# Optimization experiments

Measured on AMD Instinct MI355X. Metric: run time of the kernel, lower is better.

## Reference

```python
import jax, jax.numpy as jnp
import numpy as np

B, N, M, DQ, DK, DV, H = 8, 1024, 1024, 512, 512, 512, 8
DS = DV // H  # dim_split = 64
NEG = -1e38


def _ln(x, g, b, eps=1e-5):
    mu = jnp.mean(x, -1, keepdims=True)
    var = jnp.mean((x - mu) ** 2, -1, keepdims=True)
    return (x - mu) * jax.lax.rsqrt(var + eps) * g + b


def setup_inputs() -> dict:
    key = jax.random.key(0)
    ks = jax.random.split(key, 16)
    s = 0.02
    return {
        "x": jax.random.normal(ks[0], (B, N, DQ), jnp.float32),
        "y": jax.random.normal(ks[1], (B, M, DK), jnp.float32),
        "x_mask": jax.random.randint(ks[2], (B, N), 0, 2).astype(bool),
        "y_mask": jax.random.randint(ks[3], (B, M), 0, 2).astype(bool),
        "Wq": jax.random.normal(ks[4], (DQ, DV), jnp.float32) * s,
        "Wk": jax.random.normal(ks[5], (DK, DV), jnp.float32) * s,
        "Wv": jax.random.normal(ks[6], (DK, DV), jnp.float32) * s,
        "Wo": jax.random.normal(ks[7], (DV, DQ), jnp.float32) * s,
        "W1": jax.random.normal(ks[8], (DQ, DQ), jnp.float32) * s,
        "b1": jnp.zeros((DQ,), jnp.float32),
        "W2": jax.random.normal(ks[9], (DQ, DQ), jnp.float32) * s,
        "b2": jnp.zeros((DQ,), jnp.float32),
        "g1": jnp.ones((DQ,), jnp.float32),
        "be1": jnp.zeros((DQ,), jnp.float32),
        "g2": jnp.ones((DQ,), jnp.float32),
        "be2": jnp.zeros((DQ,), jnp.float32),
    }


def reference(x, y, x_mask, y_mask, Wq, Wk, Wv, Wo, W1, b1, W2, b2, g1, be1, g2, be2):
    xm = x_mask[..., None]  # [B,N,1]
    ym = y_mask[..., None]  # [B,M,1]
    x = jnp.where(xm, 0.0, x)
    y = jnp.where(ym, 0.0, y)
    # projections (no bias); masked rows stay zero, re-mask as in source
    q = jnp.where(xm, 0.0, x @ Wq).reshape(B, N, H, DS)
    k = jnp.where(ym, 0.0, y @ Wk).reshape(B, M, H, DS)
    v = jnp.where(ym, 0.0, y @ Wv).reshape(B, M, H, DS)
    # scaled dot product; NOTE: scale is sqrt(dim_v), faithful to source
    sdp = jnp.einsum('bnhd,bmhd->bhnm', q, k) / np.sqrt(DV)
    mask = x_mask[:, None, :, None] | y_mask[:, None, None, :]  # [B,1,N,M]
    sdp = jnp.where(mask, NEG, sdp)
    alpha = jax.nn.softmax(sdp, axis=-1)  # softmax over keys (slot_att=False)
    att = jnp.einsum('bhnm,bmhd->bnhd', alpha, v).reshape(B, N, DV)
    att = jnp.where(xm, 0.0, att)
    o = x + att @ Wo
    o = _ln(o, g1, be1)
    ff = jax.nn.relu(o @ W1 + b1) @ W2 + b2
    o = _ln(o + ff, g2, be2)
    return jnp.where(xm, 0.0, o)
```

## Files before the change

kernel.cpp:

```cpp
#include <hip/hip_runtime.h>
#include <hip/hip_bf16.h>

typedef __bf16 bf16;
typedef __attribute__((ext_vector_type(4))) __bf16 bf16x4;
typedef __attribute__((ext_vector_type(8))) __bf16 bf16x8;
typedef __attribute__((ext_vector_type(4))) float f32x4;

#define B_ 8
#define N_ 1024
#define M_ 1024
#define H_ 8
#define ROWS_ (B_ * N_)

__device__ __forceinline__ f32x4 mfma16(bf16x8 a, bf16x8 b, f32x4 c) {
    return __builtin_amdgcn_mfma_f32_16x16x32_bf16(a, b, c, 0, 0, 0);
}

__device__ __forceinline__ void glds16(const void* g, void* l) {
    __builtin_amdgcn_global_load_lds((const __attribute__((address_space(1))) void*)g,
                                     (__attribute__((address_space(3))) void*)l, 16, 0, 0);
}

__global__ __launch_bounds__(256) void prep(const float* __restrict__ x, const float* __restrict__ y,
                                            bf16* __restrict__ Xb, bf16* __restrict__ Yb,
                                            const float* W0, const float* W1, const float* W2,
                                            const float* W3, const float* W4, const float* W5,
                                            bf16* T0, bf16* T1, bf16* T2, bf16* T3, bf16* T4, bf16* T5) {
    __shared__ float t[64][65];
    int bid = blockIdx.x;
    if (bid < 8192) {
        int i = bid * 256 + threadIdx.x;
        const float4* s;
        bf16x4* d;
        int j;
        if (i < 1048576) { s = (const float4*)x; d = (bf16x4*)Xb; j = i; }
        else             { s = (const float4*)y; d = (bf16x4*)Yb; j = i - 1048576; }
        float4 f = s[j];
        bf16x4 o = {(bf16)f.x, (bf16)f.y, (bf16)f.z, (bf16)f.w};
        d[j] = o;
        return;
    }
    int wb = bid - 8192;
    const float* srcs[6] = {W0, W1, W2, W3, W4, W5};
    bf16* dsts[6] = {T0, T1, T2, T3, T4, T5};
    const float* W = srcs[wb >> 6];
    bf16* Wt = dsts[wb >> 6];
    int tile = wb & 63;
    int k0 = (tile >> 3) * 64, n0 = (tile & 7) * 64;
    int tx = threadIdx.x & 63, ty = threadIdx.x >> 6;
#pragma unroll
    for (int j = 0; j < 16; ++j)
        t[ty + j * 4][tx] = W[(size_t)(k0 + ty + j * 4) * 512 + n0 + tx];
    __syncthreads();
#pragma unroll
    for (int j = 0; j < 16; ++j)
        Wt[(size_t)(n0 + ty + j * 4) * 512 + k0 + tx] = (bf16)t[tx][ty + j * 4];
}

__device__ __forceinline__ void gemm_core(const bf16* __restrict__ A, const bf16* __restrict__ Bt,
                                          int row0, int col0, char* AsB, char* BsB, f32x4 acc[2][4]) {
    int tid = threadIdx.x, wave = tid >> 6, lane = tid & 63;
    int lr = lane & 15, q4 = lane >> 4;
    int rbase = (wave & 3) * 32, cbase = (wave >> 2) * 64;
    const bf16 *Asrc[2], *Bsrc[2];
#pragma unroll
    for (int s = 0; s < 2; ++s) {
        int c = tid + s * 512, r = c >> 3, bk = (c & 7) ^ (r & 7);
        Asrc[s] = A + (size_t)(row0 + r) * 512 + bk * 8;
        Bsrc[s] = Bt + (size_t)(col0 + r) * 512 + bk * 8;
    }
    int wb = wave * 1024;
#pragma unroll
    for (int s = 0; s < 2; ++s) {
        glds16(Asrc[s], AsB + s * 8192 + wb);
        glds16(Bsrc[s], BsB + s * 8192 + wb);
    }
#pragma unroll
    for (int it = 0; it < 8; ++it) {
        __syncthreads();
        const char* Ac = AsB + (it & 1) * 16384;
        const char* Bc = BsB + (it & 1) * 16384;
        if (it < 7) {
            char* An = AsB + ((it + 1) & 1) * 16384;
            char* Bn = BsB + ((it + 1) & 1) * 16384;
            int k0 = (it + 1) * 64;
#pragma unroll
            for (int s = 0; s < 2; ++s) {
                glds16(Asrc[s] + k0, An + s * 8192 + wb);
                glds16(Bsrc[s] + k0, Bn + s * 8192 + wb);
            }
        }
        bf16x8 af[2][2], bfr[4][2];
#pragma unroll
        for (int rt = 0; rt < 2; ++rt) {
            int row = rbase + rt * 16 + lr;
#pragma unroll
            for (int c = 0; c < 2; ++c)
                af[rt][c] = *(const bf16x8*)(Ac + (row * 8 + ((c * 4 + q4) ^ (row & 7))) * 16);
        }
#pragma unroll
        for (int ct = 0; ct < 4; ++ct) {
            int col = cbase + ct * 16 + lr;
#pragma unroll
            for (int c = 0; c < 2; ++c)
                bfr[ct][c] = *(const bf16x8*)(Bc + (col * 8 + ((c * 4 + q4) ^ (col & 7))) * 16);
        }
#pragma unroll
        for (int rt = 0; rt < 2; ++rt)
#pragma unroll
            for (int ct = 0; ct < 4; ++ct) {
                acc[rt][ct] = mfma16(af[rt][0], bfr[ct][0], acc[rt][ct]);
                acc[rt][ct] = mfma16(af[rt][1], bfr[ct][1], acc[rt][ct]);
            }
    }
}

__global__ __launch_bounds__(512, 2) void proj_qkv(const bf16* __restrict__ Xb, const bf16* __restrict__ Yb,
                                                   const bf16* __restrict__ Wqt, const bf16* __restrict__ Wkt,
                                                   const bf16* __restrict__ Wvt,
                                                   bf16* __restrict__ qb, bf16* __restrict__ kb,
                                                   bf16* __restrict__ Vt) {
    __shared__ char AsB[2 * 16384];
    __shared__ char BsB[2 * 16384];
    int z = blockIdx.z;
    const bf16 *A, *Bt;
    int row0, col0;
    if (z == 0)      { A = Xb;  Bt = Wqt; row0 = blockIdx.x * 128; col0 = blockIdx.y * 128; }
    else if (z == 1) { A = Yb;  Bt = Wkt; row0 = blockIdx.x * 128; col0 = blockIdx.y * 128; }
    else             { A = Wvt; Bt = Yb;  row0 = blockIdx.y * 128; col0 = blockIdx.x * 128; }
    const f32x4 z4 = {0.f, 0.f, 0.f, 0.f};
    f32x4 acc[2][4] = {{z4, z4, z4, z4}, {z4, z4, z4, z4}};
    gemm_core(A, Bt, row0, col0, AsB, BsB, acc);
    int wave = threadIdx.x >> 6, lane = threadIdx.x & 63, lr = lane & 15, q4 = lane >> 4;
    int rbase = (wave & 3) * 32, cbase = (wave >> 2) * 64;
    bf16* dst = (z == 0) ? qb : kb;
    const float cl = 0.06376373228f;
    float sc = (z == 0) ? cl : 1.0f;
#pragma unroll
    for (int rt = 0; rt < 2; ++rt)
#pragma unroll
        for (int ct = 0; ct < 4; ++ct) {
            int col = col0 + cbase + ct * 16 + lr;
#pragma unroll
            for (int r = 0; r < 4; ++r) {
                int row = row0 + rbase + rt * 16 + q4 * 4 + r;
                bf16 v = (bf16)(acc[rt][ct][r] * sc);
                if (z < 2) dst[(size_t)row * 512 + col] = v;
                else Vt[(size_t)((col >> 10) * 512 + row) * 1024 + (col & 1023)] = v;
            }
        }
}

template <int BIAS, int RELU>
__global__ __launch_bounds__(512, 2) void gemm_bt(const bf16* __restrict__ A, const bf16* __restrict__ Bt,
                                                  const float* __restrict__ bias, bf16* __restrict__ Cout) {
    __shared__ char AsB[2 * 16384];
    __shared__ char BsB[2 * 16384];
    int row0 = blockIdx.x * 128, col0 = blockIdx.y * 128;
    const f32x4 z4 = {0.f, 0.f, 0.f, 0.f};
    f32x4 acc[2][4] = {{z4, z4, z4, z4}, {z4, z4, z4, z4}};
    gemm_core(A, Bt, row0, col0, AsB, BsB, acc);
    int wave = threadIdx.x >> 6, lane = threadIdx.x & 63, lr = lane & 15, q4 = lane >> 4;
    int rbase = (wave & 3) * 32, cbase = (wave >> 2) * 64;
#pragma unroll
    for (int rt = 0; rt < 2; ++rt)
#pragma unroll
        for (int ct = 0; ct < 4; ++ct) {
            int col = col0 + cbase + ct * 16 + lr;
            float bv = BIAS ? bias[col] : 0.0f;
#pragma unroll
            for (int r = 0; r < 4; ++r) {
                int row = row0 + rbase + rt * 16 + q4 * 4 + r;
                float v = acc[rt][ct][r] + bv;
                if (RELU) v = fmaxf(v, 0.0f);
                Cout[(size_t)row * 512 + col] = (bf16)v;
            }
        }
}

__global__ __launch_bounds__(512, 2) void attn(const bf16* __restrict__ Q, const bf16* __restrict__ Kb,
                                               const bf16* __restrict__ Vt, const int* __restrict__ ymask,
                                               bf16* __restrict__ att) {
    __shared__ bf16 Ks[2][64 * 64];
    __shared__ bf16 Vs[2][64 * 64];
    __shared__ bf16 Ps[8][16 * 72];
    __shared__ float fmk[1024];

    int bid = blockIdx.x;
    int bh = bid & 63, n0 = (bid >> 6) * 128;
    int b = bh >> 3, h = bh & 7;
    int tid = threadIdx.x, wave = tid >> 6, lane = tid & 63;
    int lr = lane & 15, q4 = lane >> 4;

    const int* ymb = ymask + (b << 10);
    fmk[tid]       = ymb[tid]       ? -1e38f : 0.0f;
    fmk[tid + 512] = ymb[tid + 512] ? -1e38f : 0.0f;

    const bf16* qp = Q + (size_t)((b << 10) + n0 + wave * 16 + lr) * 512 + h * 64 + q4 * 8;
    bf16x8 aq0 = *(const bf16x8*)qp;
    bf16x8 aq1 = *(const bf16x8*)(qp + 32);

    bf16 one1 = (bf16)1.0f;
    bf16x8 ones = {one1, one1, one1, one1, one1, one1, one1, one1};

    int r = tid >> 3, bk = (tid & 7) ^ (r & 7);
    const bf16* Ksrc = Kb + (size_t)((b << 10) + r) * 512 + h * 64 + bk * 8;
    const bf16* Vsrc = Vt + (size_t)(b * 512 + h * 64 + r) * 1024 + bk * 8;
    int ldso = tid * 16;

    const f32x4 zv = {0.f, 0.f, 0.f, 0.f};
    f32x4 O[4] = {zv, zv, zv, zv};
    f32x4 O4 = zv;

    glds16(Ksrc, (char*)Ks[0] + ldso);
    glds16(Vsrc, (char*)Vs[0] + ldso);

    for (int it = 0; it < 16; ++it) {
        __syncthreads();
        const char* K_ = (const char*)Ks[it & 1];
        const char* V_ = (const char*)Vs[it & 1];
        if (it < 15) {
            size_t m1 = (size_t)(it + 1) * 64;
            glds16(Ksrc + m1 * 512, (char*)Ks[(it + 1) & 1] + ldso);
            glds16(Vsrc + m1, (char*)Vs[(it + 1) & 1] + ldso);
        }

#pragma unroll
        for (int nt = 0; nt < 4; ++nt) {
            int krow = nt * 16 + lr;
            bf16x8 kf0 = *(const bf16x8*)(K_ + (krow * 8 + (q4 ^ (krow & 7))) * 16);
            bf16x8 kf1 = *(const bf16x8*)(K_ + (krow * 8 + ((4 + q4) ^ (krow & 7))) * 16);
            float fm = fmk[it * 64 + krow];
            f32x4 s = {fm, fm, fm, fm};
            s = mfma16(aq0, kf0, s);
            s = mfma16(aq1, kf1, s);
#pragma unroll
            for (int rr = 0; rr < 4; ++rr)
                Ps[wave][(q4 * 4 + rr) * 72 + krow] = (bf16)exp2f(s[rr]);
        }
        bf16x8 ap0 = *(const bf16x8*)&Ps[wave][lr * 72 + q4 * 8];
        bf16x8 ap1 = *(const bf16x8*)&Ps[wave][lr * 72 + 32 + q4 * 8];
        O4 = mfma16(ap0, ones, O4);
        O4 = mfma16(ap1, ones, O4);
#pragma unroll
        for (int dt = 0; dt < 4; ++dt) {
            int vrow = dt * 16 + lr;
            bf16x8 vf0 = *(const bf16x8*)(V_ + (vrow * 8 + (q4 ^ (vrow & 7))) * 16);
            bf16x8 vf1 = *(const bf16x8*)(V_ + (vrow * 8 + ((4 + q4) ^ (vrow & 7))) * 16);
            O[dt] = mfma16(ap0, vf0, O[dt]);
            O[dt] = mfma16(ap1, vf1, O[dt]);
        }
    }

    float inv[4];
#pragma unroll
    for (int rr = 0; rr < 4; ++rr)
        inv[rr] = (O4[rr] > 0.0f) ? (1.0f / O4[rr]) : 0.0f;
#pragma unroll
    for (int dt = 0; dt < 4; ++dt)
#pragma unroll
        for (int rr = 0; rr < 4; ++rr) {
            int row = n0 + wave * 16 + q4 * 4 + rr;
            att[(size_t)((b << 10) + row) * 512 + h * 64 + dt * 16 + lr] =
                (bf16)(O[dt][rr] * inv[rr]);
        }
}

__global__ __launch_bounds__(128) void ln1_k(const float* __restrict__ X, const bf16* __restrict__ A,
                                             const float* __restrict__ g, const float* __restrict__ be,
                                             bf16* __restrict__ Obf) {
    int row = blockIdx.x, t = threadIdx.x;
    float4 xv = ((const float4*)(X + (size_t)row * 512))[t];
    bf16x4 av = ((const bf16x4*)(A + (size_t)row * 512))[t];
    float4 o = {xv.x + (float)av.x, xv.y + (float)av.y, xv.z + (float)av.z, xv.w + (float)av.w};
    float s = o.x + o.y + o.z + o.w;
    float sq = o.x * o.x + o.y * o.y + o.z * o.z + o.w * o.w;
#pragma unroll
    for (int off = 1; off < 64; off <<= 1) { s += __shfl_xor(s, off); sq += __shfl_xor(sq, off); }
    __shared__ float ls[2], lq[2];
    if ((t & 63) == 0) { ls[t >> 6] = s; lq[t >> 6] = sq; }
    __syncthreads();
    s = ls[0] + ls[1]; sq = lq[0] + lq[1];
    float mu = s * (1.0f / 512.0f);
    float var = sq * (1.0f / 512.0f) - mu * mu;
    float rs = rsqrtf(var + 1e-5f);
    float4 gv = ((const float4*)g)[t];
    float4 bv = ((const float4*)be)[t];
    bf16x4 b4 = {(bf16)((o.x - mu) * rs * gv.x + bv.x), (bf16)((o.y - mu) * rs * gv.y + bv.y),
                 (bf16)((o.z - mu) * rs * gv.z + bv.z), (bf16)((o.w - mu) * rs * gv.w + bv.w)};
    ((bf16x4*)(Obf + (size_t)row * 512))[t] = b4;
}

__global__ __launch_bounds__(128) void ln2_k(const bf16* __restrict__ Ob, const bf16* __restrict__ F,
                                             const float* __restrict__ g, const float* __restrict__ be,
                                             const int* __restrict__ xmask, float* __restrict__ out) {
    int row = blockIdx.x, t = threadIdx.x;
    bf16x4 xv = ((const bf16x4*)(Ob + (size_t)row * 512))[t];
    bf16x4 rv = ((const bf16x4*)(F + (size_t)row * 512))[t];
    float4 o = {(float)xv.x + (float)rv.x, (float)xv.y + (float)rv.y,
                (float)xv.z + (float)rv.z, (float)xv.w + (float)rv.w};
    float s = o.x + o.y + o.z + o.w;
    float sq = o.x * o.x + o.y * o.y + o.z * o.z + o.w * o.w;
#pragma unroll
    for (int off = 1; off < 64; off <<= 1) { s += __shfl_xor(s, off); sq += __shfl_xor(sq, off); }
    __shared__ float ls[2], lq[2];
    if ((t & 63) == 0) { ls[t >> 6] = s; lq[t >> 6] = sq; }
    __syncthreads();
    s = ls[0] + ls[1]; sq = lq[0] + lq[1];
    float mu = s * (1.0f / 512.0f);
    float var = sq * (1.0f / 512.0f) - mu * mu;
    float rs = rsqrtf(var + 1e-5f);
    int msk = xmask[row];
    float4 gv = ((const float4*)g)[t];
    float4 bv = ((const float4*)be)[t];
    float4 r4 = {(o.x - mu) * rs * gv.x + bv.x, (o.y - mu) * rs * gv.y + bv.y,
                 (o.z - mu) * rs * gv.z + bv.z, (o.w - mu) * rs * gv.w + bv.w};
    if (msk) r4 = {0.f, 0.f, 0.f, 0.f};
    ((float4*)(out + (size_t)row * 512))[t] = r4;
}

extern "C" void kernel_launch(void* const* d_in, const int* in_sizes, int n_in,
                              void* d_out, int out_size, void* d_ws, size_t ws_size,
                              hipStream_t stream) {
    const float* x   = (const float*)d_in[0];
    const float* y   = (const float*)d_in[1];
    const int*   xm  = (const int*)d_in[2];
    const int*   ym  = (const int*)d_in[3];
    const float* Wq  = (const float*)d_in[4];
    const float* Wk  = (const float*)d_in[5];
    const float* Wv  = (const float*)d_in[6];
    const float* Wo  = (const float*)d_in[7];
    const float* W1  = (const float*)d_in[8];
    const float* b1  = (const float*)d_in[9];
    const float* W2  = (const float*)d_in[10];
    const float* b2  = (const float*)d_in[11];
    const float* g1  = (const float*)d_in[12];
    const float* be1 = (const float*)d_in[13];
    const float* g2  = (const float*)d_in[14];
    const float* be2 = (const float*)d_in[15];

    char* ws = (char*)d_ws;
    const size_t WT_SZ  = 512 * 512 * sizeof(bf16);
    const size_t XB_SZ  = (size_t)ROWS_ * 512 * sizeof(bf16);

    bf16* Wqt = (bf16*)(ws + 0 * WT_SZ);
    bf16* Wkt = (bf16*)(ws + 1 * WT_SZ);
    bf16* Wvt = (bf16*)(ws + 2 * WT_SZ);
    bf16* Wot = (bf16*)(ws + 3 * WT_SZ);
    bf16* W1t = (bf16*)(ws + 4 * WT_SZ);
    bf16* W2t = (bf16*)(ws + 5 * WT_SZ);
    size_t off = 6 * WT_SZ;
    bf16* Xb  = (bf16*)(ws + off); off += XB_SZ;
    bf16* Yb  = (bf16*)(ws + off); off += XB_SZ;
    bf16* qb  = (bf16*)(ws + off); off += XB_SZ;
    bf16* kb  = (bf16*)(ws + off); off += XB_SZ;
    bf16* Vt  = (bf16*)(ws + off); off += XB_SZ;
    bf16* attb = Xb;
    bf16* awo  = kb;
    bf16* obf  = qb;
    bf16* hb   = Yb;
    bf16* fb   = Vt;

    prep<<<8576, 256, 0, stream>>>(x, y, Xb, Yb, Wq, Wk, Wv, Wo, W1, W2,
                                   Wqt, Wkt, Wvt, Wot, W1t, W2t);

    proj_qkv<<<dim3(64, 4, 3), 512, 0, stream>>>(Xb, Yb, Wqt, Wkt, Wvt, qb, kb, Vt);

    attn<<<512, 512, 0, stream>>>(qb, kb, Vt, ym, attb);

    dim3 gg(64, 4);
    gemm_bt<0, 0><<<gg, 512, 0, stream>>>(attb, Wot, nullptr, awo);
    ln1_k<<<ROWS_, 128, 0, stream>>>(x, awo, g1, be1, obf);
    gemm_bt<1, 1><<<gg, 512, 0, stream>>>(obf, W1t, b1, hb);
    gemm_bt<1, 0><<<gg, 512, 0, stream>>>(hb, W2t, b2, fb);
    ln2_k<<<ROWS_, 128, 0, stream>>>(obf, fb, g2, be2, xm, (float*)d_out);
}
```

Before: 213.1 us.

## Process two query row tiles per wave in attention to reuse K/V fragments

```diff
diff --git a/kernel.cpp b/kernel.cpp
--- a/kernel.cpp
+++ b/kernel.cpp
@@ -178,12 +178,12 @@
         }
 }
 
-__global__ __launch_bounds__(512, 2) void attn(const bf16* __restrict__ Q, const bf16* __restrict__ Kb,
+__global__ __launch_bounds__(256, 2) void attn(const bf16* __restrict__ Q, const bf16* __restrict__ Kb,
                                                const bf16* __restrict__ Vt, const int* __restrict__ ymask,
                                                bf16* __restrict__ att) {
     __shared__ bf16 Ks[2][64 * 64];
     __shared__ bf16 Vs[2][64 * 64];
-    __shared__ bf16 Ps[8][16 * 72];
+    __shared__ bf16 Ps[4][32 * 72];
     __shared__ float fmk[1024];
 
     int bid = blockIdx.x;
@@ -193,27 +193,45 @@
     int lr = lane & 15, q4 = lane >> 4;
 
     const int* ymb = ymask + (b << 10);
-    fmk[tid]       = ymb[tid]       ? -1e38f : 0.0f;
-    fmk[tid + 512] = ymb[tid + 512] ? -1e38f : 0.0f;
-
-    const bf16* qp = Q + (size_t)((b << 10) + n0 + wave * 16 + lr) * 512 + h * 64 + q4 * 8;
-    bf16x8 aq0 = *(const bf16x8*)qp;
-    bf16x8 aq1 = *(const bf16x8*)(qp + 32);
+#pragma unroll
+    for (int j = 0; j < 4; ++j) {
+        int i = tid + j * 256;
+        fmk[i] = ymb[i] ? -1e38f : 0.0f;
+    }
+
+    bf16x8 aq[2][2];
+#pragma unroll
+    for (int rt = 0; rt < 2; ++rt) {
+        const bf16* qp = Q + (size_t)((b << 10) + n0 + wave * 32 + rt * 16 + lr) * 512 + h * 64 + q4 * 8;
+        aq[rt][0] = *(const bf16x8*)qp;
+        aq[rt][1] = *(const bf16x8*)(qp + 32);
+    }
 
     bf16 one1 = (bf16)1.0f;
     bf16x8 ones = {one1, one1, one1, one1, one1, one1, one1, one1};
 
-    int r = tid >> 3, bk = (tid & 7) ^ (r & 7);
-    const bf16* Ksrc = Kb + (size_t)((b << 10) + r) * 512 + h * 64 + bk * 8;
-    const bf16* Vsrc = Vt + (size_t)(b * 512 + h * 64 + r) * 1024 + bk * 8;
-    int ldso = tid * 16;
+    const bf16 *Ksrc[2], *Vsrc[2];
+#pragma unroll
+    for (int s = 0; s < 2; ++s) {
+        int c = tid + s * 256, r = c >> 3, bk = (c & 7) ^ (r & 7);
+        Ksrc[s] = Kb + (size_t)((b << 10) + r) * 512 + h * 64 + bk * 8;
+        Vsrc[s] = Vt + (size_t)(b * 512 + h * 64 + r) * 1024 + bk * 8;
+    }
+    int wb = wave * 1024;
 
     const f32x4 zv = {0.f, 0.f, 0.f, 0.f};
-    f32x4 O[4] = {zv, zv, zv, zv};
-    f32x4 O4 = zv;
-
-    glds16(Ksrc, (char*)Ks[0] + ldso);
-    glds16(Vsrc, (char*)Vs[0] + ldso);
+    f32x4 O[2][4];
+    f32x4 O4[2] = {zv, zv};
+#pragma unroll
+    for (int rt = 0; rt < 2; ++rt)
+#pragma unroll
+        for (int dt = 0; dt < 4; ++dt) O[rt][dt] = zv;
+
+#pragma unroll
+    for (int s = 0; s < 2; ++s) {
+        glds16(Ksrc[s], (char*)Ks[0] + s * 4096 + wb);
+        glds16(Vsrc[s], (char*)Vs[0] + s * 4096 + wb);
+    }
 
     for (int it = 0; it < 16; ++it) {
         __syncthreads();
@@ -221,8 +239,11 @@
         const char* V_ = (const char*)Vs[it & 1];
         if (it < 15) {
             size_t m1 = (size_t)(it + 1) * 64;
-            glds16(Ksrc + m1 * 512, (char*)Ks[(it + 1) & 1] + ldso);
-            glds16(Vsrc + m1, (char*)Vs[(it + 1) & 1] + ldso);
+#pragma unroll
+            for (int s = 0; s < 2; ++s) {
+                glds16(Ksrc[s] + m1 * 512, (char*)Ks[(it + 1) & 1] + s * 4096 + wb);
+                glds16(Vsrc[s] + m1, (char*)Vs[(it + 1) & 1] + s * 4096 + wb);
+            }
         }
 
 #pragma unroll
@@ -231,39 +252,52 @@
             bf16x8 kf0 = *(const bf16x8*)(K_ + (krow * 8 + (q4 ^ (krow & 7))) * 16);
             bf16x8 kf1 = *(const bf16x8*)(K_ + (krow * 8 + ((4 + q4) ^ (krow & 7))) * 16);
             float fm = fmk[it * 64 + krow];
-            f32x4 s = {fm, fm, fm, fm};
-            s = mfma16(aq0, kf0, s);
-            s = mfma16(aq1, kf1, s);
-#pragma unroll
-            for (int rr = 0; rr < 4; ++rr)
-                Ps[wave][(q4 * 4 + rr) * 72 + krow] = (bf16)exp2f(s[rr]);
-        }
-        bf16x8 ap0 = *(const bf16x8*)&Ps[wave][lr * 72 + q4 * 8];
-        bf16x8 ap1 = *(const bf16x8*)&Ps[wave][lr * 72 + 32 + q4 * 8];
-        O4 = mfma16(ap0, ones, O4);
-        O4 = mfma16(ap1, ones, O4);
+            f32x4 cinit = {fm, fm, fm, fm};
+#pragma unroll
+            for (int rt = 0; rt < 2; ++rt) {
+                f32x4 s = mfma16(aq[rt][0], kf0, cinit);
+                s = mfma16(aq[rt][1], kf1, s);
+#pragma unroll
+                for (int rr = 0; rr < 4; ++rr)
+                    Ps[wave][(rt * 16 + q4 * 4 + rr) * 72 + krow] = (bf16)exp2f(s[rr]);
+            }
+        }
+        bf16x8 ap[2][2];
+#pragma unroll
+        for (int rt = 0; rt < 2; ++rt) {
+            ap[rt][0] = *(const bf16x8*)&Ps[wave][(rt * 16 + lr) * 72 + q4 * 8];
+            ap[rt][1] = *(const bf16x8*)&Ps[wave][(rt * 16 + lr) * 72 + 32 + q4 * 8];
+            O4[rt] = mfma16(ap[rt][0], ones, O4[rt]);
+            O4[rt] = mfma16(ap[rt][1], ones, O4[rt]);
+        }
 #pragma unroll
         for (int dt = 0; dt < 4; ++dt) {
             int vrow = dt * 16 + lr;
             bf16x8 vf0 = *(const bf16x8*)(V_ + (vrow * 8 + (q4 ^ (vrow & 7))) * 16);
             bf16x8 vf1 = *(const bf16x8*)(V_ + (vrow * 8 + ((4 + q4) ^ (vrow & 7))) * 16);
-            O[dt] = mfma16(ap0, vf0, O[dt]);
-            O[dt] = mfma16(ap1, vf1, O[dt]);
-        }
-    }
-
-    float inv[4];
-#pragma unroll
-    for (int rr = 0; rr < 4; ++rr)
-        inv[rr] = (O4[rr] > 0.0f) ? (1.0f / O4[rr]) : 0.0f;
-#pragma unroll
-    for (int dt = 0; dt < 4; ++dt)
-#pragma unroll
-        for (int rr = 0; rr < 4; ++rr) {
-            int row = n0 + wave * 16 + q4 * 4 + rr;
-            att[(size_t)((b << 10) + row) * 512 + h * 64 + dt * 16 + lr] =
-                (bf16)(O[dt][rr] * inv[rr]);
-        }
+#pragma unroll
+            for (int rt = 0; rt < 2; ++rt) {
+                O[rt][dt] = mfma16(ap[rt][0], vf0, O[rt][dt]);
+                O[rt][dt] = mfma16(ap[rt][1], vf1, O[rt][dt]);
+            }
+        }
+    }
+
+#pragma unroll
+    for (int rt = 0; rt < 2; ++rt) {
+        float inv[4];
+#pragma unroll
+        for (int rr = 0; rr < 4; ++rr)
+            inv[rr] = (O4[rt][rr] > 0.0f) ? (1.0f / O4[rt][rr]) : 0.0f;
+#pragma unroll
+        for (int dt = 0; dt < 4; ++dt)
+#pragma unroll
+            for (int rr = 0; rr < 4; ++rr) {
+                int row = n0 + wave * 32 + rt * 16 + q4 * 4 + rr;
+                att[(size_t)((b << 10) + row) * 512 + h * 64 + dt * 16 + lr] =
+                    (bf16)(O[rt][dt][rr] * inv[rr]);
+            }
+    }
 }
 
 __global__ __launch_bounds__(128) void ln1_k(const float* __restrict__ X, const bf16* __restrict__ A,
@@ -366,7 +400,7 @@
 
     proj_qkv<<<dim3(64, 4, 3), 512, 0, stream>>>(Xb, Yb, Wqt, Wkt, Wvt, qb, kb, Vt);
 
-    attn<<<512, 512, 0, stream>>>(qb, kb, Vt, ym, attb);
+    attn<<<512, 256, 0, stream>>>(qb, kb, Vt, ym, attb);
 
     dim3 gg(64, 4);
     gemm_bt<0, 0><<<gg, 512, 0, stream>>>(attb, Wot, nullptr, awo);
```

After: 215.0 us. No clear change (+0.9%).
